# Kernel tuning notes

Hardware: AMD Instinct MI355X
Metric: run time of the kernel (lower is better)

The kernel has to match this reference:

```python
import jax, jax.numpy as jnp
import numpy as np

B, L, C, H, W = 8, 8, 64, 56, 56
K = 3
EPS = 1e-5


def setup_inputs() -> dict:
    key = jax.random.key(0)
    ks = jax.random.split(key, 7)
    s = lambda k, shape, sc=0.05: jax.random.normal(k, shape, dtype=jnp.float32) * sc
    return {
        "x": jax.random.normal(ks[0], (B, L, C, H, W), dtype=jnp.float32),
        "temporal_w": s(ks[1], (C, C)),        # Conv3d 1x1x1 C->C
        "temporal_b": s(ks[2], (C,)),
        "fc_w": s(ks[3], (C,)),                # Conv3d 1x1x1 C->1
        "fc_b": s(ks[4], (1,)),
        "conv_w": s(ks[5], (C, C, K, K), 0.1), # self.weight [1,1,Co,Ci,k,k] core
        "conv_b": s(ks[6], (C,)),              # self.bias [1,1,Co] core
        "bn_gamma": jnp.ones((C,), jnp.float32),
        "bn_beta": jnp.zeros((C,), jnp.float32),
    }


def reference(x, temporal_w, temporal_b, fc_w, fc_b, conv_w, conv_b, bn_gamma, bn_beta):
    b, l, c, h, w = x.shape
    # ---- generateweight_fourier ----
    xin = jnp.transpose(x, (0, 2, 1, 3, 4))                # [B,C,L,H,W]
    f = jnp.fft.fft2(xin, axes=(3, 4), norm='ortho')       # spatial FFT
    f = jnp.fft.fft(f, axis=2, norm='ortho')               # temporal FFT
    allxin = xin + 0.01 * jnp.abs(f) * xin                 # Fourier2 attention + residual
    pooled = allxin.mean(axis=(3, 4))                      # AdaptiveAvgPool3d((None,1,1)) -> [B,C,L]
    # temporalconv: 1x1x1 Conv3d C->C on [B,C,L,1,1]
    calib = jnp.einsum('oc,bcl->bol', temporal_w, pooled) + temporal_b[None, :, None]  # [B,C,L]
    # fc: 1x1x1 Conv3d C->1
    fcout = jnp.einsum('c,bcl->bl', fc_w, pooled) + fc_b[0]                            # [B,L]
    # finalweight: weight[1,1,Co,Ci,k,k] * (calib+1) broadcast over Ci -> [B,L,Co,Ci,k,k]
    calib_blc = jnp.transpose(calib, (0, 2, 1)) + 1.0      # [B,L,Ci]
    fw = conv_w[None, None] * calib_blc[:, :, None, :, None, None]
    fb = conv_b[None, None, :] * (fcout + 1.0)[:, :, None] # [B,L,Co]
    # ---- dynamic per-(sample,frame) conv2d (groups = b*l) ----
    x_flat = x.reshape(b * l, c, h, w)
    fw_flat = fw.reshape(b * l, c, c, K, K)
    fb_flat = fb.reshape(b * l, c)

    def per_sample(xi, wi):
        return jax.lax.conv_general_dilated(
            xi[None], wi, window_strides=(1, 1), padding=[(1, 1), (1, 1)],
            dimension_numbers=('NCHW', 'OIHW', 'NCHW'))[0]

    out = jax.vmap(per_sample)(x_flat, fw_flat) + fb_flat[:, :, None, None]
    out = x_flat + out                                     # residual (gate=False)
    # BatchNorm2d (training-mode batch statistics)
    mean = out.mean(axis=(0, 2, 3), keepdims=True)
    var = out.var(axis=(0, 2, 3), keepdims=True)
    out = (out - mean) * jax.lax.rsqrt(var + EPS)
    out = out * bn_gamma[None, :, None, None] + bn_beta[None, :, None, None]
    out = out * jax.nn.sigmoid(out)                        # SiLU
    return out.reshape(b, l, c, h, w)
```

## Files before the change

kernel.cpp:

```cpp
#include <hip/hip_runtime.h>
#include <cmath>

#define HW 3136
#define NF 64
#define NBLK2 448

typedef __attribute__((ext_vector_type(8))) short short8;
typedef __attribute__((ext_vector_type(4))) float float4a;

__device__ __forceinline__ unsigned short f2bf(float f) {
    unsigned int u = __float_as_uint(f);
    u += 0x7fffu + ((u >> 16) & 1u);
    return (unsigned short)(u >> 16);
}
__device__ __forceinline__ float bf2f(unsigned short u) {
    return __uint_as_float(((unsigned int)u) << 16);
}

__global__ __launch_bounds__(256)
void pack_kernel(const float* __restrict__ cw,
                 unsigned short* __restrict__ Ffix,
                 unsigned short* __restrict__ Wp) {
    if (blockIdx.x < 64) {
        int idx = blockIdx.x * 256 + threadIdx.x;
        int j    = idx & 7;
        int lane = (idx >> 3) & 63;
        int ks   = (idx >> 9) & 3;
        int t    = (idx >> 11) & 3;
        int p    = (idx >> 13) & 1;
        int mn = t * 16 + (lane & 15);
        int k  = ks * 32 + (lane >> 4) * 8 + j;
        float val = 0.f;
        if (mn < 56 && k < 112) {
            int h = k >> 1;
            int prod = (mn * h) % 56;
            float ang = -6.2831853071795864f * (float)prod / 56.0f;
            float cr = cosf(ang);
            float ci = sinf(ang);
            if (p == 0) val = (k & 1) ? -ci : cr;
            else        val = (k & 1) ?  cr : ci;
        }
        Ffix[idx] = f2bf(val);
    } else {
        int idx = (blockIdx.x - 64) * 256 + threadIdx.x;
        if (idx < 36864) {
            int i  = idx & 63;
            int o  = (idx >> 6) & 63;
            int kk = idx >> 12;
            Wp[idx] = f2bf(cw[(o * 64 + i) * 9 + kk]);
        }
    }
}

__global__ __launch_bounds__(256, 2)
void fft_mfma_kernel(const float* __restrict__ x,
                     const unsigned short* __restrict__ Ffix,
                     float* __restrict__ pooled) {
    const int bc = blockIdx.x;
    const int c  = bc & 63;
    const int b  = bc >> 6;
    const int tid  = threadIdx.x;
    const int lane = tid & 63;
    const int wv   = tid >> 6;
    const int n    = lane & 15;
    const int q    = lane >> 4;

    __shared__ unsigned short sh[40320];
    unsigned short* xbf = sh;
    unsigned short* Tb  = sh + 25088;
    unsigned short* Ub  = sh + 25088 + 56 * 136;
    __shared__ float xsum[8];
    __shared__ float red[8];

    for (int t = tid; t < 7616; t += 256)
        ((unsigned int*)(sh + 25088))[t] = 0u;

    for (int t = tid; t < 6272; t += 256) {
        int l = t / 784, r = t - l * 784;
        float4 v = *(const float4*)(x + ((size_t)((b * 8 + l) * 64 + c)) * HW + r * 4);
        ushort4 o;
        o.x = f2bf(v.x); o.y = f2bf(v.y); o.z = f2bf(v.z); o.w = f2bf(v.w);
        *(ushort4*)(xbf + l * 3136 + r * 4) = o;
    }
    __syncthreads();

    {
        float s0 = 0.f, s4 = 0.f;
        for (int i = lane; i < 3136; i += 64) {
            s0 += bf2f(xbf[wv * 3136 + i]);
            s4 += bf2f(xbf[(wv + 4) * 3136 + i]);
        }
        #pragma unroll
        for (int m = 1; m < 64; m <<= 1) {
            s0 += __shfl_xor(s0, m);
            s4 += __shfl_xor(s4, m);
        }
        if (lane == 0) { xsum[wv] = s0; xsum[wv + 4] = s4; }
    }

    #pragma unroll 1
    for (int lp = 0; lp < 5; ++lp) {
        float tr[8], ti[8];
        #pragma unroll
        for (int l = 0; l < 8; ++l) {
            float ang = -0.78539816339744831f * (float)((l * lp) & 7);
            tr[l] = cosf(ang);
            ti[l] = sinf(ang);
        }
        for (int s = tid; s < 784; s += 256) {
            int h = s / 14, w4 = s - h * 14;
            float re[4] = {0.f, 0.f, 0.f, 0.f}, im[4] = {0.f, 0.f, 0.f, 0.f};
            #pragma unroll
            for (int l = 0; l < 8; ++l) {
                ushort4 u = *(const ushort4*)(xbf + l * 3136 + h * 56 + w4 * 4);
                float v0 = bf2f(u.x), v1 = bf2f(u.y), v2 = bf2f(u.z), v3 = bf2f(u.w);
                re[0] += v0 * tr[l]; im[0] += v0 * ti[l];
                re[1] += v1 * tr[l]; im[1] += v1 * ti[l];
                re[2] += v2 * tr[l]; im[2] += v2 * ti[l];
                re[3] += v3 * tr[l]; im[3] += v3 * ti[l];
            }
            #pragma unroll
            for (int jj = 0; jj < 4; ++jj) {
                int j = (jj + w4) & 3;
                int w = w4 * 4 + j;
                unsigned int pk = (unsigned int)f2bf(re[j])
                                | ((unsigned int)f2bf(im[j]) << 16);
                ((unsigned int*)Tb)[w * 68 + h] = pk;
            }
        }
        __syncthreads();

        {
            const int p  = wv >> 1;
            const int mh = (wv & 1) * 2;
            float4a s1[2][4];
            #pragma unroll
            for (int mi = 0; mi < 2; ++mi)
                #pragma unroll
                for (int nt = 0; nt < 4; ++nt) s1[mi][nt] = (float4a){0.f, 0.f, 0.f, 0.f};
            #pragma unroll
            for (int ks = 0; ks < 4; ++ks) {
                short8 bfr[4];
                #pragma unroll
                for (int nt = 0; nt < 4; ++nt) {
                    int row = nt * 16 + n; if (row > 55) row = 55;
                    bfr[nt] = *(const short8*)(Tb + row * 136 + ks * 32 + q * 8);
                }
                #pragma unroll
                for (int mi = 0; mi < 2; ++mi) {
                    short8 afr = *(const short8*)(Ffix + ((((p * 4 + mh + mi) * 4 + ks) * 64 + lane) * 8));
                    #pragma unroll
                    for (int nt = 0; nt < 4; ++nt)
                        s1[mi][nt] = __builtin_amdgcn_mfma_f32_16x16x32_bf16(afr, bfr[nt], s1[mi][nt], 0, 0, 0);
                }
            }
            #pragma unroll
            for (int mi = 0; mi < 2; ++mi)
                #pragma unroll
                for (int nt = 0; nt < 4; ++nt)
                    #pragma unroll
                    for (int r = 0; r < 4; ++r) {
                        int kh = (mh + mi) * 16 + q * 4 + r;
                        int w  = nt * 16 + n;
                        if (kh < 56 && w < 56)
                            Ub[kh * 136 + 2 * w + p] = f2bf(s1[mi][nt][r]);
                    }
        }
        __syncthreads();

        const int mt = wv;
        short8 afr2[4];
        #pragma unroll
        for (int ks = 0; ks < 4; ++ks) {
            int row = mt * 16 + n; if (row > 55) row = 55;
            afr2[ks] = *(const short8*)(Ub + row * 136 + ks * 32 + q * 8);
        }
        float4a g[2][4];
        #pragma unroll
        for (int pp = 0; pp < 2; ++pp)
            #pragma unroll
            for (int nt = 0; nt < 4; ++nt) g[pp][nt] = (float4a){0.f, 0.f, 0.f, 0.f};
        #pragma unroll
        for (int pp = 0; pp < 2; ++pp)
            #pragma unroll
            for (int ks = 0; ks < 4; ++ks)
                #pragma unroll
                for (int nt = 0; nt < 4; ++nt) {
                    short8 bfr = *(const short8*)(Ffix + ((((pp * 4 + nt) * 4 + ks) * 64 + lane) * 8));
                    g[pp][nt] = __builtin_amdgcn_mfma_f32_16x16x32_bf16(afr2[ks], bfr, g[pp][nt], 0, 0, 0);
                }

        const bool doflip = (lp >= 1 && lp <= 3);
        const unsigned short* x1 = xbf + lp * 3136;
        const unsigned short* x2 = xbf + ((8 - lp) & 7) * 3136;
        float S1 = 0.f, S2 = 0.f;
        #pragma unroll
        for (int nt = 0; nt < 4; ++nt) {
            int kw = nt * 16 + n;
            if (kw < 56) {
                int kwf = (56 - kw) % 56;
                #pragma unroll
                for (int r = 0; r < 4; ++r) {
                    int kh = mt * 16 + q * 4 + r;
                    if (kh < 56) {
                        float gr = g[0][nt][r], gi = g[1][nt][r];
                        float mag = sqrtf(gr * gr + gi * gi);
                        S1 += mag * bf2f(x1[kh * 56 + kw]);
                        if (doflip) {
                            int khf = (56 - kh) % 56;
                            S2 += mag * bf2f(x2[khf * 56 + kwf]);
                        }
                    }
                }
            }
        }
        #pragma unroll
        for (int m = 1; m < 64; m <<= 1) {
            S1 += __shfl_xor(S1, m);
            S2 += __shfl_xor(S2, m);
        }
        if (lane == 0) { red[wv * 2] = S1; red[wv * 2 + 1] = S2; }
        __syncthreads();
        if (tid == 0) {
            float s1 = 0.f, s2 = 0.f;
            #pragma unroll
            for (int w = 0; w < 4; ++w) { s1 += red[w * 2]; s2 += red[w * 2 + 1]; }
            const float kS = 0.01f / (56.0f * 2.8284271247461903f);
            pooled[bc * 8 + lp] = (xsum[lp] + kS * s1) / 3136.0f;
            if (doflip)
                pooled[bc * 8 + (8 - lp)] = (xsum[8 - lp] + kS * s2) / 3136.0f;
        }
    }
}

__global__ __launch_bounds__(64)
void calib_kernel(const float* __restrict__ pooled,
                  const float* __restrict__ tw_, const float* __restrict__ tb,
                  const float* __restrict__ fcw, const float* __restrict__ fcb,
                  const float* __restrict__ convb,
                  float* __restrict__ scale, float* __restrict__ fbias) {
    const int nn = blockIdx.x;
    const int b = nn >> 3, l = nn & 7;
    const int o = threadIdx.x;
    const float* pr = pooled + b * 512 + l;
    float dot = 0.f;
    #pragma unroll 8
    for (int c0 = 0; c0 < 64; ++c0) dot += tw_[o * 64 + c0] * pr[c0 * 8];
    float fcp = fcw[o] * pr[o * 8];
    #pragma unroll
    for (int off = 32; off > 0; off >>= 1) fcp += __shfl_down(fcp, off);
    float fcout = __shfl(fcp, 0) + fcb[0];
    scale[nn * 64 + o] = 1.0f + tb[o] + dot;
    fbias[nn * 64 + o] = convb[o] * (fcout + 1.0f);
}

__global__ __launch_bounds__(256, 2)
void conv_mfma_kernel(const float* __restrict__ x,
                      const unsigned short* __restrict__ Wp,
                      const float* __restrict__ scale, const float* __restrict__ fbias,
                      float* __restrict__ out,
                      float* __restrict__ psum, float* __restrict__ psum2) {
    const int rt = blockIdx.x;
    const int nn = blockIdx.y;
    const int tid  = threadIdx.x;
    const int lane = tid & 63;
    const int wv   = tid >> 6;
    const int r0   = rt * 8;

    __shared__ unsigned short xs[10 * 60 * 64];
    __shared__ float fb[64], ssc[64], rsc[64], bn1[64], bn2[64];

    if (tid < 64) {
        fb[tid]  = fbias[nn * 64 + tid];
        float s  = scale[nn * 64 + tid];
        ssc[tid] = s;
        rsc[tid] = 1.0f / s;
        bn1[tid] = 0.f; bn2[tid] = 0.f;
    }
    __syncthreads();

    for (int t = tid; t < 10240; t += 256) {
        if (t < 8960) {
            int c4 = t % 14;
            int rr = (t / 14) % 10;
            int i  = t / 140;
            int gr = r0 - 1 + rr;
            float4 v = make_float4(0.f, 0.f, 0.f, 0.f);
            if (gr >= 0 && gr < 56)
                v = *(const float4*)(x + ((size_t)(nn * 64 + i) * HW + gr * 56 + c4 * 4));
            float s = ssc[i];
            int g = i >> 3, il = i & 7;
            float vv[4] = {v.x, v.y, v.z, v.w};
            #pragma unroll
            for (int j = 0; j < 4; ++j) {
                int lc = c4 * 4 + 1 + j;
                xs[(rr * 60 + lc) * 64 + (((g ^ (lc & 7)) << 3) | il)] = f2bf(vv[j] * s);
            }
        } else {
            int idx = t - 8960;
            int i   = idx / 20;
            int rem = idx - i * 20;
            int rr  = rem >> 1;
            int lc  = (rem & 1) * 57;
            int g = i >> 3, il = i & 7;
            xs[(rr * 60 + lc) * 64 + (((g ^ (lc & 7)) << 3) | il)] = 0;
        }
    }
    __syncthreads();

    const int pxo = lane & 15;
    const int q   = lane >> 4;

    float4a acc[7][4];
    #pragma unroll
    for (int j = 0; j < 7; ++j)
        #pragma unroll
        for (int ot = 0; ot < 4; ++ot) acc[j][ot] = (float4a){0.f, 0.f, 0.f, 0.f};

    int rp[7], cp[7];
    #pragma unroll
    for (int j = 0; j < 7; ++j) {
        int px = (wv * 7 + j) * 16 + pxo;
        rp[j] = px / 56;
        cp[j] = px - rp[j] * 56;
    }

    #pragma unroll 1
    for (int kk = 0; kk < 9; ++kk) {
        const int dr = kk / 3, dc = kk - dr * 3;
        short8 a[4][2];
        #pragma unroll
        for (int ot = 0; ot < 4; ++ot)
            #pragma unroll
            for (int ih = 0; ih < 2; ++ih)
                a[ot][ih] = *(const short8*)(Wp + ((kk * 64 + ot * 16 + pxo) * 64 + ih * 32 + q * 8));

        #pragma unroll
        for (int j = 0; j < 7; ++j) {
            int lc = cp[j] + dc;
            int base = ((rp[j] + dr) * 60 + lc) * 64;
            int sw = lc & 7;
            #pragma unroll
            for (int ih = 0; ih < 2; ++ih) {
                short8 bv = *(const short8*)&xs[base + (((q + ih * 4) ^ sw) << 3)];
                #pragma unroll
                for (int ot = 0; ot < 4; ++ot)
                    acc[j][ot] = __builtin_amdgcn_mfma_f32_16x16x32_bf16(a[ot][ih], bv, acc[j][ot], 0, 0, 0);
            }
        }
    }

    float bs[4][4], bs2[4][4];
    #pragma unroll
    for (int ot = 0; ot < 4; ++ot)
        #pragma unroll
        for (int r = 0; r < 4; ++r) { bs[ot][r] = 0.f; bs2[ot][r] = 0.f; }

    #pragma unroll
    for (int j = 0; j < 7; ++j) {
        int px  = (wv * 7 + j) * 16 + pxo;
        int gpx = r0 * 56 + px;
        int rr  = rp[j] + 1;
        int lc  = cp[j] + 1;
        int sw  = lc & 7;
        int rowbase = (rr * 60 + lc) * 64;
        #pragma unroll
        for (int ot = 0; ot < 4; ++ot) {
            int g  = ot * 2 + (q >> 1);
            ushort4 uu = *(const ushort4*)(xs + rowbase + (((g ^ sw) << 3) | ((q & 1) * 4)));
            float resid[4] = {bf2f(uu.x), bf2f(uu.y), bf2f(uu.z), bf2f(uu.w)};
            #pragma unroll
            for (int r = 0; r < 4; ++r) {
                int o = ot * 16 + q * 4 + r;
                size_t off = (size_t)(nn * 64 + o) * HW + gpx;
                float v = acc[j][ot][r] + resid[r] * rsc[o] + fb[o];
                out[off] = v;
                bs[ot][r]  += v;
                bs2[ot][r] += v * v;
            }
        }
    }
    #pragma unroll
    for (int ot = 0; ot < 4; ++ot)
        #pragma unroll
        for (int r = 0; r < 4; ++r) {
            #pragma unroll
            for (int m = 1; m < 16; m <<= 1) {
                bs[ot][r]  += __shfl_xor(bs[ot][r], m);
                bs2[ot][r] += __shfl_xor(bs2[ot][r], m);
            }
        }
    if (pxo == 0) {
        #pragma unroll
        for (int ot = 0; ot < 4; ++ot)
            #pragma unroll
            for (int r = 0; r < 4; ++r) {
                int o = ot * 16 + q * 4 + r;
                atomicAdd(&bn1[o], bs[ot][r]);
                atomicAdd(&bn2[o], bs2[ot][r]);
            }
    }
    __syncthreads();
    if (tid < 64) {
        int bl = nn * 7 + rt;
        psum[bl * 64 + tid]  = bn1[tid];
        psum2[bl * 64 + tid] = bn2[tid];
    }
}

__global__ __launch_bounds__(256)
void bnstat_kernel(const float* __restrict__ psum, const float* __restrict__ psum2,
                   float* __restrict__ bn) {
    const int o = blockIdx.x;
    const int tid = threadIdx.x;
    float s = 0.f, s2 = 0.f;
    for (int bl = tid; bl < NBLK2; bl += 256) {
        s  += psum[bl * 64 + o];
        s2 += psum2[bl * 64 + o];
    }
    __shared__ float r1[256], r2[256];
    r1[tid] = s; r2[tid] = s2;
    __syncthreads();
    for (int st = 128; st > 0; st >>= 1) {
        if (tid < st) { r1[tid] += r1[tid + st]; r2[tid] += r2[tid + st]; }
        __syncthreads();
    }
    if (tid == 0) {
        const float N = 64.0f * (float)HW;
        float mean = r1[0] / N;
        float var  = r2[0] / N - mean * mean;
        bn[o]      = mean;
        bn[64 + o] = rsqrtf(var + 1e-5f);
    }
}

__global__ __launch_bounds__(256)
void bnsilu_kernel(float* __restrict__ out, const float* __restrict__ bn,
                   const float* __restrict__ gamma, const float* __restrict__ beta) {
    size_t idx = (size_t)blockIdx.x * 256 + threadIdx.x;
    if (idx >= (size_t)NF * 64 * HW) return;
    int c = (int)((idx / HW) & 63);
    float v = out[idx];
    float y = (v - bn[c]) * bn[64 + c] * gamma[c] + beta[c];
    out[idx] = y / (1.0f + expf(-y));
}

extern "C" void kernel_launch(void* const* d_in, const int* in_sizes, int n_in,
                              void* d_out, int out_size, void* d_ws, size_t ws_size,
                              hipStream_t stream) {
    const float* x          = (const float*)d_in[0];
    const float* temporal_w = (const float*)d_in[1];
    const float* temporal_b = (const float*)d_in[2];
    const float* fc_w       = (const float*)d_in[3];
    const float* fc_b       = (const float*)d_in[4];
    const float* conv_w     = (const float*)d_in[5];
    const float* conv_b     = (const float*)d_in[6];
    const float* bn_gamma   = (const float*)d_in[7];
    const float* bn_beta    = (const float*)d_in[8];
    float* out = (float*)d_out;
    float* ws  = (float*)d_ws;

    float* pooled = ws;
    float* scale  = ws + 4096;
    float* fbias  = ws + 8192;
    unsigned short* Wp = (unsigned short*)(ws + 12288);
    float* psum   = ws + 12288 + 18432;
    float* psum2  = psum + NBLK2 * 64;
    float* bn     = psum2 + NBLK2 * 64;
    unsigned short* Ffix = (unsigned short*)(bn + 128);

    pack_kernel<<<208, 256, 0, stream>>>(conv_w, Ffix, Wp);
    fft_mfma_kernel<<<512, 256, 0, stream>>>(x, Ffix, pooled);
    calib_kernel<<<64, 64, 0, stream>>>(pooled, temporal_w, temporal_b,
                                        fc_w, fc_b, conv_b, scale, fbias);
    conv_mfma_kernel<<<dim3(7, 64), 256, 0, stream>>>(x, Wp, scale, fbias,
                                                      out, psum, psum2);
    bnstat_kernel<<<64, 256, 0, stream>>>(psum, psum2, bn);
    int total = NF * 64 * HW;
    bnsilu_kernel<<<(total + 255) / 256, 256, 0, stream>>>(out, bn, bn_gamma, bn_beta);
}
```

Measured before the change: 232.2 us.

## Split Fourier attention into per-frame 2D DFT and a temporal-combine kernel

Replaces the single fused FFT kernel, which looped over five temporal frequencies per (b,c) block, with a per-(b,c,l) spatial 2D DFT kernel that uses MFMA on a real-input half-spectrum (29 rows, exploiting Hermitian symmetry). A separate combine kernel applies the 8-point temporal DFT in registers, takes the magnitude, and accumulates against x and its mirrored positions to produce pooled values. This raises parallelism from 512 blocks to 4096 and removes the repeated spatial transforms per temporal frequency. In exchange, the intermediate spectrum makes a global round trip through the output buffer used as scratch, and x is reread from global memory in the combine step.

```diff
diff --git a/kernel.cpp b/kernel.cpp
--- a/kernel.cpp
+++ b/kernel.cpp
@@ -4,6 +4,8 @@
 #define HW 3136
 #define NF 64
 #define NBLK2 448
+#define YROWS 29
+#define YPX 1624
 
 typedef __attribute__((ext_vector_type(8))) short short8;
 typedef __attribute__((ext_vector_type(4))) float float4a;
@@ -20,7 +22,8 @@
 __global__ __launch_bounds__(256)
 void pack_kernel(const float* __restrict__ cw,
                  unsigned short* __restrict__ Ffix,
-                 unsigned short* __restrict__ Wp) {
+                 unsigned short* __restrict__ Wp,
+                 unsigned short* __restrict__ Fs1) {
     if (blockIdx.x < 64) {
         int idx = blockIdx.x * 256 + threadIdx.x;
         int j    = idx & 7;
@@ -41,7 +44,7 @@
             else        val = (k & 1) ?  cr : ci;
         }
         Ffix[idx] = f2bf(val);
-    } else {
+    } else if (blockIdx.x < 208) {
         int idx = (blockIdx.x - 64) * 256 + threadIdx.x;
         if (idx < 36864) {
             int i  = idx & 63;
@@ -49,14 +52,37 @@
             int kk = idx >> 12;
             Wp[idx] = f2bf(cw[(o * 64 + i) * 9 + kk]);
         }
-    }
-}
-
-__global__ __launch_bounds__(256, 2)
-void fft_mfma_kernel(const float* __restrict__ x,
-                     const unsigned short* __restrict__ Ffix,
-                     float* __restrict__ pooled) {
-    const int bc = blockIdx.x;
+    } else {
+        int idx = (blockIdx.x - 208) * 256 + threadIdx.x;
+        int j  = idx & 7;
+        int ln = (idx >> 3) & 63;
+        int ks = (idx >> 9) & 1;
+        int mt = (idx >> 10) & 3;
+        int m = mt * 16 + (ln & 15);
+        int k = ks * 32 + (ln >> 4) * 8 + j;
+        float val = 0.f;
+        if (k < 56) {
+            if (m < 29) {
+                int prod = (m * k) % 56;
+                val = cosf(-6.2831853071795864f * (float)prod / 56.0f);
+            } else if (m >= 32 && m < 61) {
+                int mm = m - 32;
+                int prod = (mm * k) % 56;
+                val = sinf(-6.2831853071795864f * (float)prod / 56.0f);
+            }
+        }
+        Fs1[idx] = f2bf(val);
+    }
+}
+
+__global__ __launch_bounds__(256)
+void dft2d_kernel(const float* __restrict__ x,
+                  const unsigned short* __restrict__ Fs1,
+                  const unsigned short* __restrict__ Ffix,
+                  unsigned short* __restrict__ Y) {
+    const int bid = blockIdx.x;
+    const int l  = bid & 7;
+    const int bc = bid >> 3;
     const int c  = bc & 63;
     const int b  = bc >> 6;
     const int tid  = threadIdx.x;
@@ -65,171 +91,163 @@
     const int n    = lane & 15;
     const int q    = lane >> 4;
 
-    __shared__ unsigned short sh[40320];
-    unsigned short* xbf = sh;
-    unsigned short* Tb  = sh + 25088;
-    unsigned short* Ub  = sh + 25088 + 56 * 136;
-    __shared__ float xsum[8];
-    __shared__ float red[8];
-
-    for (int t = tid; t < 7616; t += 256)
-        ((unsigned int*)(sh + 25088))[t] = 0u;
-
-    for (int t = tid; t < 6272; t += 256) {
-        int l = t / 784, r = t - l * 784;
-        float4 v = *(const float4*)(x + ((size_t)((b * 8 + l) * 64 + c)) * HW + r * 4);
-        ushort4 o;
-        o.x = f2bf(v.x); o.y = f2bf(v.y); o.z = f2bf(v.z); o.w = f2bf(v.w);
-        *(ushort4*)(xbf + l * 3136 + r * 4) = o;
+    __shared__ unsigned short xT[64 * 68];
+    __shared__ unsigned short P[32 * 136];
+
+    for (int t = tid; t < 656; t += 256) {
+        if (t < 384) ((unsigned int*)xT)[(t / 6) * 34 + 28 + (t % 6)] = 0u;
+        else         ((unsigned int*)xT)[56 * 34 + (t - 384)] = 0u;
+    }
+    const float* xp = x + ((size_t)((b * 8 + l) * 64 + c)) * HW;
+    for (int t = tid; t < 784; t += 256) {
+        int h = t / 14, w4 = t - h * 14;
+        float4 v = *(const float4*)(xp + h * 56 + w4 * 4);
+        xT[(w4 * 4 + 0) * 68 + h] = f2bf(v.x);
+        xT[(w4 * 4 + 1) * 68 + h] = f2bf(v.y);
+        xT[(w4 * 4 + 2) * 68 + h] = f2bf(v.z);
+        xT[(w4 * 4 + 3) * 68 + h] = f2bf(v.w);
     }
     __syncthreads();
 
     {
-        float s0 = 0.f, s4 = 0.f;
-        for (int i = lane; i < 3136; i += 64) {
-            s0 += bf2f(xbf[wv * 3136 + i]);
-            s4 += bf2f(xbf[(wv + 4) * 3136 + i]);
-        }
-        #pragma unroll
-        for (int m = 1; m < 64; m <<= 1) {
-            s0 += __shfl_xor(s0, m);
-            s4 += __shfl_xor(s4, m);
-        }
-        if (lane == 0) { xsum[wv] = s0; xsum[wv + 4] = s4; }
-    }
-
-    #pragma unroll 1
-    for (int lp = 0; lp < 5; ++lp) {
-        float tr[8], ti[8];
-        #pragma unroll
-        for (int l = 0; l < 8; ++l) {
-            float ang = -0.78539816339744831f * (float)((l * lp) & 7);
-            tr[l] = cosf(ang);
-            ti[l] = sinf(ang);
-        }
-        for (int s = tid; s < 784; s += 256) {
-            int h = s / 14, w4 = s - h * 14;
-            float re[4] = {0.f, 0.f, 0.f, 0.f}, im[4] = {0.f, 0.f, 0.f, 0.f};
-            #pragma unroll
-            for (int l = 0; l < 8; ++l) {
-                ushort4 u = *(const ushort4*)(xbf + l * 3136 + h * 56 + w4 * 4);
-                float v0 = bf2f(u.x), v1 = bf2f(u.y), v2 = bf2f(u.z), v3 = bf2f(u.w);
-                re[0] += v0 * tr[l]; im[0] += v0 * ti[l];
-                re[1] += v1 * tr[l]; im[1] += v1 * ti[l];
-                re[2] += v2 * tr[l]; im[2] += v2 * ti[l];
-                re[3] += v3 * tr[l]; im[3] += v3 * ti[l];
-            }
-            #pragma unroll
-            for (int jj = 0; jj < 4; ++jj) {
-                int j = (jj + w4) & 3;
-                int w = w4 * 4 + j;
-                unsigned int pk = (unsigned int)f2bf(re[j])
-                                | ((unsigned int)f2bf(im[j]) << 16);
-                ((unsigned int*)Tb)[w * 68 + h] = pk;
-            }
-        }
-        __syncthreads();
-
-        {
-            const int p  = wv >> 1;
-            const int mh = (wv & 1) * 2;
-            float4a s1[2][4];
-            #pragma unroll
-            for (int mi = 0; mi < 2; ++mi)
+        float4a acc[4];
+        #pragma unroll
+        for (int nt = 0; nt < 4; ++nt) acc[nt] = (float4a){0.f, 0.f, 0.f, 0.f};
+        #pragma unroll
+        for (int ks = 0; ks < 2; ++ks) {
+            short8 afr = *(const short8*)(Fs1 + ((size_t)((wv * 2 + ks) * 64 + lane)) * 8);
+            #pragma unroll
+            for (int nt = 0; nt < 4; ++nt) {
+                short8 bfr = *(const short8*)(xT + (nt * 16 + n) * 68 + ks * 32 + q * 8);
+                acc[nt] = __builtin_amdgcn_mfma_f32_16x16x32_bf16(afr, bfr, acc[nt], 0, 0, 0);
+            }
+        }
+        #pragma unroll
+        for (int nt = 0; nt < 4; ++nt)
+            #pragma unroll
+            for (int r = 0; r < 4; ++r) {
+                int m = wv * 16 + q * 4 + r;
+                P[(m & 31) * 136 + 2 * (nt * 16 + n) + (m >> 5)] = f2bf(acc[nt][r]);
+            }
+    }
+    __syncthreads();
+
+    {
+        const int p  = wv >> 1;
+        const int ch = wv & 1;
+        short8 afr[2][4];
+        #pragma unroll
+        for (int mt = 0; mt < 2; ++mt)
+            #pragma unroll
+            for (int ks = 0; ks < 4; ++ks)
+                afr[mt][ks] = *(const short8*)(P + (mt * 16 + n) * 136 + ks * 32 + q * 8);
+        float4a acc[2][2];
+        #pragma unroll
+        for (int mt = 0; mt < 2; ++mt)
+            #pragma unroll
+            for (int u = 0; u < 2; ++u) acc[mt][u] = (float4a){0.f, 0.f, 0.f, 0.f};
+        #pragma unroll
+        for (int ks = 0; ks < 4; ++ks)
+            #pragma unroll
+            for (int u = 0; u < 2; ++u) {
+                int nt = ch * 2 + u;
+                short8 bfr = *(const short8*)(Ffix + ((size_t)(((p * 4 + nt) * 4 + ks) * 64 + lane)) * 8);
                 #pragma unroll
-                for (int nt = 0; nt < 4; ++nt) s1[mi][nt] = (float4a){0.f, 0.f, 0.f, 0.f};
-            #pragma unroll
-            for (int ks = 0; ks < 4; ++ks) {
-                short8 bfr[4];
-                #pragma unroll
-                for (int nt = 0; nt < 4; ++nt) {
-                    int row = nt * 16 + n; if (row > 55) row = 55;
-                    bfr[nt] = *(const short8*)(Tb + row * 136 + ks * 32 + q * 8);
-                }
-                #pragma unroll
-                for (int mi = 0; mi < 2; ++mi) {
-                    short8 afr = *(const short8*)(Ffix + ((((p * 4 + mh + mi) * 4 + ks) * 64 + lane) * 8));
-                    #pragma unroll
-                    for (int nt = 0; nt < 4; ++nt)
-                        s1[mi][nt] = __builtin_amdgcn_mfma_f32_16x16x32_bf16(afr, bfr[nt], s1[mi][nt], 0, 0, 0);
-                }
-            }
-            #pragma unroll
-            for (int mi = 0; mi < 2; ++mi)
-                #pragma unroll
-                for (int nt = 0; nt < 4; ++nt)
-                    #pragma unroll
-                    for (int r = 0; r < 4; ++r) {
-                        int kh = (mh + mi) * 16 + q * 4 + r;
-                        int w  = nt * 16 + n;
-                        if (kh < 56 && w < 56)
-                            Ub[kh * 136 + 2 * w + p] = f2bf(s1[mi][nt][r]);
-                    }
-        }
-        __syncthreads();
-
-        const int mt = wv;
-        short8 afr2[4];
-        #pragma unroll
-        for (int ks = 0; ks < 4; ++ks) {
-            int row = mt * 16 + n; if (row > 55) row = 55;
-            afr2[ks] = *(const short8*)(Ub + row * 136 + ks * 32 + q * 8);
-        }
-        float4a g[2][4];
-        #pragma unroll
-        for (int pp = 0; pp < 2; ++pp)
-            #pragma unroll
-            for (int nt = 0; nt < 4; ++nt) g[pp][nt] = (float4a){0.f, 0.f, 0.f, 0.f};
-        #pragma unroll
-        for (int pp = 0; pp < 2; ++pp)
-            #pragma unroll
-            for (int ks = 0; ks < 4; ++ks)
-                #pragma unroll
-                for (int nt = 0; nt < 4; ++nt) {
-                    short8 bfr = *(const short8*)(Ffix + ((((pp * 4 + nt) * 4 + ks) * 64 + lane) * 8));
-                    g[pp][nt] = __builtin_amdgcn_mfma_f32_16x16x32_bf16(afr2[ks], bfr, g[pp][nt], 0, 0, 0);
-                }
-
-        const bool doflip = (lp >= 1 && lp <= 3);
-        const unsigned short* x1 = xbf + lp * 3136;
-        const unsigned short* x2 = xbf + ((8 - lp) & 7) * 3136;
-        float S1 = 0.f, S2 = 0.f;
-        #pragma unroll
-        for (int nt = 0; nt < 4; ++nt) {
-            int kw = nt * 16 + n;
-            if (kw < 56) {
-                int kwf = (56 - kw) % 56;
+                for (int mt = 0; mt < 2; ++mt)
+                    acc[mt][u] = __builtin_amdgcn_mfma_f32_16x16x32_bf16(afr[mt][ks], bfr, acc[mt][u], 0, 0, 0);
+            }
+        unsigned short* Yo = Y + ((size_t)bid * 2 + p) * YPX;
+        #pragma unroll
+        for (int mt = 0; mt < 2; ++mt)
+            #pragma unroll
+            for (int u = 0; u < 2; ++u)
                 #pragma unroll
                 for (int r = 0; r < 4; ++r) {
-                    int kh = mt * 16 + q * 4 + r;
-                    if (kh < 56) {
-                        float gr = g[0][nt][r], gi = g[1][nt][r];
-                        float mag = sqrtf(gr * gr + gi * gi);
-                        S1 += mag * bf2f(x1[kh * 56 + kw]);
-                        if (doflip) {
-                            int khf = (56 - kh) % 56;
-                            S2 += mag * bf2f(x2[khf * 56 + kwf]);
-                        }
-                    }
+                    int row = mt * 16 + q * 4 + r;
+                    int col = (ch * 2 + u) * 16 + n;
+                    if (row < YROWS && col < 56)
+                        Yo[row * 56 + col] = f2bf(acc[mt][u][r]);
                 }
-            }
-        }
+    }
+}
+
+__global__ __launch_bounds__(256)
+void combine_kernel(const float* __restrict__ x,
+                    const unsigned short* __restrict__ Y,
+                    float* __restrict__ pooled) {
+    const int bc = blockIdx.x;
+    const int c  = bc & 63;
+    const int b  = bc >> 6;
+    const int tid  = threadIdx.x;
+    const int lane = tid & 63;
+    const int wv   = tid >> 6;
+
+    const float SQH = 0.70710678118654752f;
+    const float c8[8] = {1.f,  SQH, 0.f, -SQH, -1.f, -SQH, 0.f,  SQH};
+    const float s8[8] = {0.f, -SQH, -1.f, -SQH, 0.f,  SQH, 1.f,  SQH};
+
+    float S[8], X[8];
+    #pragma unroll
+    for (int i = 0; i < 8; ++i) { S[i] = 0.f; X[i] = 0.f; }
+
+    const size_t xbase = ((size_t)(b * 8) * 64 + c) * HW;
+    const unsigned short* Yb = Y + (size_t)bc * 16 * YPX;
+
+    for (int t = tid; t < YPX; t += 256) {
+        int kh = t / 56, kw = t - kh * 56;
+        float Yr[8], Yi[8];
+        #pragma unroll
+        for (int l = 0; l < 8; ++l) {
+            Yr[l] = bf2f(Yb[(l * 2 + 0) * YPX + t]);
+            Yi[l] = bf2f(Yb[(l * 2 + 1) * YPX + t]);
+        }
+        float mag[8];
+        #pragma unroll
+        for (int tt = 0; tt < 8; ++tt) {
+            float gr = 0.f, gi = 0.f;
+            #pragma unroll
+            for (int l = 0; l < 8; ++l) {
+                const int k = (tt * l) & 7;
+                gr += c8[k] * Yr[l] - s8[k] * Yi[l];
+                gi += c8[k] * Yi[l] + s8[k] * Yr[l];
+            }
+            mag[tt] = sqrtf(gr * gr + gi * gi);
+        }
+        const bool mir = (kh >= 1 && kh <= 27);
+        const int tm = (56 - kh) * 56 + (kw ? 56 - kw : 0);
+        #pragma unroll
+        for (int l = 0; l < 8; ++l) {
+            float xb = x[xbase + (size_t)l * 64 * HW + t];
+            S[l] += mag[l] * xb;
+            X[l] += xb;
+            if (mir) {
+                float xm = x[xbase + (size_t)l * 64 * HW + tm];
+                S[l] += mag[(8 - l) & 7] * xm;
+                X[l] += xm;
+            }
+        }
+    }
+
+    __shared__ float red[4][16];
+    #pragma unroll
+    for (int i = 0; i < 8; ++i) {
         #pragma unroll
         for (int m = 1; m < 64; m <<= 1) {
-            S1 += __shfl_xor(S1, m);
-            S2 += __shfl_xor(S2, m);
-        }
-        if (lane == 0) { red[wv * 2] = S1; red[wv * 2 + 1] = S2; }
-        __syncthreads();
-        if (tid == 0) {
-            float s1 = 0.f, s2 = 0.f;
-            #pragma unroll
-            for (int w = 0; w < 4; ++w) { s1 += red[w * 2]; s2 += red[w * 2 + 1]; }
-            const float kS = 0.01f / (56.0f * 2.8284271247461903f);
-            pooled[bc * 8 + lp] = (xsum[lp] + kS * s1) / 3136.0f;
-            if (doflip)
-                pooled[bc * 8 + (8 - lp)] = (xsum[8 - lp] + kS * s2) / 3136.0f;
-        }
+            S[i] += __shfl_xor(S[i], m);
+            X[i] += __shfl_xor(X[i], m);
+        }
+    }
+    if (lane == 0) {
+        #pragma unroll
+        for (int i = 0; i < 8; ++i) { red[wv][i] = S[i]; red[wv][8 + i] = X[i]; }
+    }
+    __syncthreads();
+    if (tid < 8) {
+        float s = 0.f, xs = 0.f;
+        #pragma unroll
+        for (int w = 0; w < 4; ++w) { s += red[w][tid]; xs += red[w][8 + tid]; }
+        const float kS = 0.01f / (56.0f * 2.8284271247461903f);
+        pooled[bc * 8 + tid] = (xs + kS * s) / 3136.0f;
     }
 }
 
@@ -468,9 +486,13 @@
     float* psum2  = psum + NBLK2 * 64;
     float* bn     = psum2 + NBLK2 * 64;
     unsigned short* Ffix = (unsigned short*)(bn + 128);
-
-    pack_kernel<<<208, 256, 0, stream>>>(conv_w, Ffix, Wp);
-    fft_mfma_kernel<<<512, 256, 0, stream>>>(x, Ffix, pooled);
+    unsigned short* Fs1  = Ffix + 16384;
+
+    unsigned short* Y = (unsigned short*)out;
+
+    pack_kernel<<<224, 256, 0, stream>>>(conv_w, Ffix, Wp, Fs1);
+    dft2d_kernel<<<4096, 256, 0, stream>>>(x, Fs1, Ffix, Y);
+    combine_kernel<<<512, 256, 0, stream>>>(x, Y, pooled);
     calib_kernel<<<64, 64, 0, stream>>>(pooled, temporal_w, temporal_b,
                                         fc_w, fc_b, conv_b, scale, fbias);
     conv_mfma_kernel<<<dim3(7, 64), 256, 0, stream>>>(x, Wp, scale, fbias,
```

After: 235.6 us. About the same (+1.5%).
